# Optimization experiments

Measured on AMD Instinct MI355X. Metric: run time of the kernel, lower is better.

The kernel has to match this reference:

```python
import jax, jax.numpy as jnp
import numpy as np

B, H, W, C, F = 8, 128, 128, 256, 256

def setup_inputs() -> dict:
    key = jax.random.key(0)
    k1, k2, k3 = jax.random.split(key, 3)
    x = jax.random.normal(k1, (B, H, W, C), dtype=jnp.float32)
    style = jax.random.normal(k2, (B, 1, 1, C), dtype=jnp.float32)
    # he_uniform over fan_in = 3*3*C
    limit = np.sqrt(6.0 / (3 * 3 * C)).astype(np.float32)
    kernel = jax.random.uniform(k3, (3, 3, C, F), dtype=jnp.float32, minval=-limit, maxval=limit)
    return {"x": x, "style": style, "kernel": kernel}

def reference(x, style, kernel):
    b, h, w_, c = x.shape
    f = kernel.shape[-1]
    # per-sample modulation: [B,1,1,C,1] * [1,3,3,C,F] -> [B,3,3,C,F]
    wmod = kernel[None] * (style[..., None] + 1.0)
    demod = jnp.sqrt(jnp.sum(jnp.square(wmod), axis=(1, 2, 3), keepdims=True) + 1e-8)
    wmod = wmod / demod
    # grouped conv trick: x -> [1, B*C, H, W], filters -> [3,3,C,B*F], groups=B
    xg = jnp.transpose(x, (0, 3, 1, 2)).reshape(1, b * c, h, w_)
    wf = jnp.transpose(wmod, (1, 2, 3, 0, 4)).reshape(3, 3, c, b * f)
    y = jax.lax.conv_general_dilated(
        xg, wf, window_strides=(1, 1), padding='SAME',
        dimension_numbers=('NCHW', 'HWIO', 'NCHW'),
        feature_group_count=b)
    y = y.reshape(b, f, h, w_)
    return jnp.transpose(y, (0, 2, 3, 1))
```

## Files before the change

### kernel.cpp

```cpp
#include <hip/hip_runtime.h>
#include <hip/hip_bf16.h>


#define NB 8
#define NH 128
#define NW 128
#define NC 256
#define NF 256

typedef __attribute__((ext_vector_type(8))) short bf16x8;
typedef __attribute__((ext_vector_type(4))) float f32x4;

__global__ void k_cvt(const float* __restrict__ x, ushort* __restrict__ xbf) {
    int i = (blockIdx.x * blockDim.x + threadIdx.x) * 4;
    float4 v = *(const float4*)(x + i);
    union { ushort4 u; __hip_bfloat16 h[4]; } o;
    o.h[0] = __float2bfloat16(v.x);
    o.h[1] = __float2bfloat16(v.y);
    o.h[2] = __float2bfloat16(v.z);
    o.h[3] = __float2bfloat16(v.w);
    *(ushort4*)(xbf + i) = o.u;
}

__global__ void k_modw(const float* __restrict__ kern, const float* __restrict__ style,
                       ushort* __restrict__ wm) {
    int b = blockIdx.x >> 8;
    int f = blockIdx.x & 255;
    int c = threadIdx.x;
    float s = style[b * 256 + c] + 1.0f;
    float w[9];
    float acc = 0.f;
#pragma unroll
    for (int t = 0; t < 9; ++t) {
        w[t] = kern[(t * 256 + c) * 256 + f] * s;
        acc += w[t] * w[t];
    }
#pragma unroll
    for (int off = 32; off; off >>= 1) acc += __shfl_down(acc, off);
    __shared__ float part[4];
    if ((threadIdx.x & 63) == 0) part[threadIdx.x >> 6] = acc;
    __syncthreads();
    float total = part[0] + part[1] + part[2] + part[3];
    float inv = 1.0f / sqrtf(total + 1e-8f);
#pragma unroll
    for (int t = 0; t < 9; ++t) {
        union { ushort u; __hip_bfloat16 h; } o;
        o.h = __float2bfloat16(w[t] * inv);
        wm[(((b * 9 + t) * 256 + f) * 256) + c] = o.u;
    }
}

__global__ void __launch_bounds__(256)
k_conv(const ushort* __restrict__ xbf, const ushort* __restrict__ wm,
       float* __restrict__ out) {
    const int bidx = blockIdx.x;
    const int fh = bidx & 1;
    const int h  = (bidx >> 1) & 127;
    const int b  = bidx >> 8;

    __shared__ ushort As[3][130 * 32];
    __shared__ ushort Bs[128 * 32];

    const int tid = threadIdx.x;
    const int wave = tid >> 6, lane = tid & 63;
    const int wm_ = wave & 1, wn_ = wave >> 1;
    const int lrow = lane & 15;
    const int quad = lane >> 4;

    for (int i = tid; i < 3 * 2 * 32; i += 256) {
        int dh = i >> 6;
        int side = (i >> 5) & 1;
        int cc = i & 31;
        As[dh][(side ? 129 : 0) * 32 + cc] = 0;
    }
#pragma unroll
    for (int dh = 0; dh < 3; ++dh) {
        int hp = h + dh - 1;
        if (hp < 0 || hp >= 128) {
            for (int i = tid; i < 130 * 32; i += 256) As[dh][i] = 0;
        }
    }

    f32x4 acc[4][4];
    const f32x4 zero4 = {0.f, 0.f, 0.f, 0.f};
#pragma unroll
    for (int mi = 0; mi < 4; ++mi)
#pragma unroll
        for (int ni = 0; ni < 4; ++ni) acc[mi][ni] = zero4;

    const int wload = tid >> 2;
    const int cload = (tid & 3) * 8;

    for (int c0 = 0; c0 < 256; c0 += 32) {
        __syncthreads();
#pragma unroll
        for (int dh = 0; dh < 3; ++dh) {
            int hp = h + dh - 1;
            if (hp >= 0 && hp < 128) {
                const ushort* src = xbf + ((b * 128 + hp) * 128) * 256 + c0;
#pragma unroll
                for (int j = 0; j < 2; ++j) {
                    int w = j * 64 + wload;
                    uint4 v = *(const uint4*)(src + w * 256 + cload);
                    *(uint4*)&As[dh][(w + 1) * 32 + cload] = v;
                }
            }
        }
#pragma unroll
        for (int dh = 0; dh < 3; ++dh) {
#pragma unroll
            for (int dw = 0; dw < 3; ++dw) {
                const int tap = dh * 3 + dw;
                __syncthreads();
                {
                    const ushort* src = wm + ((b * 9 + tap) * 256 + fh * 128) * 256 + c0;
#pragma unroll
                    for (int j = 0; j < 2; ++j) {
                        int fl = j * 64 + wload;
                        uint4 v = *(const uint4*)(src + fl * 256 + cload);
                        *(uint4*)&Bs[fl * 32 + cload] = v;
                    }
                }
                __syncthreads();
                bf16x8 af[4], bfr[4];
#pragma unroll
                for (int ni = 0; ni < 4; ++ni) {
                    int fl = wn_ * 64 + ni * 16 + lrow;
                    bfr[ni] = *(const bf16x8*)&Bs[fl * 32 + quad * 8];
                }
#pragma unroll
                for (int mi = 0; mi < 4; ++mi) {
                    int w = wm_ * 64 + mi * 16 + lrow;
                    af[mi] = *(const bf16x8*)&As[dh][(w + dw) * 32 + quad * 8];
                }
#pragma unroll
                for (int mi = 0; mi < 4; ++mi)
#pragma unroll
                    for (int ni = 0; ni < 4; ++ni)
                        acc[mi][ni] = __builtin_amdgcn_mfma_f32_16x16x32_bf16(
                            af[mi], bfr[ni], acc[mi][ni], 0, 0, 0);
            }
        }
    }

    float* obase = out + ((b * 128 + h) * 128) * 256 + fh * 128;
#pragma unroll
    for (int mi = 0; mi < 4; ++mi) {
        int wrow = wm_ * 64 + mi * 16 + quad * 4;
#pragma unroll
        for (int ni = 0; ni < 4; ++ni) {
            int f = wn_ * 64 + ni * 16 + lrow;
            f32x4 v = acc[mi][ni];
#pragma unroll
            for (int r = 0; r < 4; ++r) {
                obase[(wrow + r) * 256 + f] = v[r];
            }
        }
    }
}

extern "C" void kernel_launch(void* const* d_in, const int* in_sizes, int n_in,
                              void* d_out, int out_size, void* d_ws, size_t ws_size,
                              hipStream_t stream) {
    const float* x     = (const float*)d_in[0];
    const float* style = (const float*)d_in[1];
    const float* kern  = (const float*)d_in[2];
    float* out = (float*)d_out;

    ushort* xbf = (ushort*)d_ws;
    ushort* wmod = xbf + (size_t)NB * NH * NW * NC;

    k_cvt<<<(NB * NH * NW * NC) / (256 * 4), 256, 0, stream>>>(x, xbf);
    k_modw<<<NB * NF, 256, 0, stream>>>(kern, style, wmod);
    k_conv<<<NB * NH * 2, 256, 0, stream>>>(xbf, wmod, out);
}
```

Before: 408.4 us.

## Double-buffer weight tiles with direct global-to-LDS loads and swizzle block order

Weight and input tiles are now loaded straight from global memory into LDS with global_load_lds, with no round trip through registers. The weight tile is double-buffered so the next tap's weights are prefetched while the current tap's MFMAs run, which roughly halves the barriers per channel chunk. Block indices are remapped so that consecutive launched blocks spread across batches, which changes which blocks run together and how they share cache. The risk is that the asynchronous LDS loads depend on the compiler inserting the right vmcnt waits before each barrier.

```diff
diff --git a/kernel.cpp b/kernel.cpp
--- a/kernel.cpp
+++ b/kernel.cpp
@@ -10,6 +10,12 @@
 
 typedef __attribute__((ext_vector_type(8))) short bf16x8;
 typedef __attribute__((ext_vector_type(4))) float f32x4;
+
+__device__ __forceinline__ void gload16(const ushort* g, ushort* l) {
+    __builtin_amdgcn_global_load_lds(
+        (const __attribute__((address_space(1))) unsigned int*)g,
+        (__attribute__((address_space(3))) unsigned int*)l, 16, 0, 0);
+}
 
 __global__ void k_cvt(const float* __restrict__ x, ushort* __restrict__ xbf) {
     int i = (blockIdx.x * blockDim.x + threadIdx.x) * 4;
@@ -53,19 +59,22 @@
 __global__ void __launch_bounds__(256)
 k_conv(const ushort* __restrict__ xbf, const ushort* __restrict__ wm,
        float* __restrict__ out) {
-    const int bidx = blockIdx.x;
+    const int bidx = (blockIdx.x & 7) * 256 + (blockIdx.x >> 3);
     const int fh = bidx & 1;
     const int h  = (bidx >> 1) & 127;
     const int b  = bidx >> 8;
 
     __shared__ ushort As[3][130 * 32];
-    __shared__ ushort Bs[128 * 32];
+    __shared__ ushort Bs[2][128 * 32];
 
     const int tid = threadIdx.x;
     const int wave = tid >> 6, lane = tid & 63;
     const int wm_ = wave & 1, wn_ = wave >> 1;
     const int lrow = lane & 15;
     const int quad = lane >> 4;
+
+    const int lw = lane >> 2;
+    const int lc = (lane & 3) * 8;
 
     for (int i = tid; i < 3 * 2 * 32; i += 256) {
         int dh = i >> 6;
@@ -88,62 +97,70 @@
 #pragma unroll
         for (int ni = 0; ni < 4; ++ni) acc[mi][ni] = zero4;
 
-    const int wload = tid >> 2;
-    const int cload = (tid & 3) * 8;
+    const ushort* wmb = wm + ((size_t)(b * 9) * 256 + fh * 128) * 256;
 
-    for (int c0 = 0; c0 < 256; c0 += 32) {
-        __syncthreads();
+    auto stageA = [&](int c0) {
 #pragma unroll
         for (int dh = 0; dh < 3; ++dh) {
             int hp = h + dh - 1;
             if (hp >= 0 && hp < 128) {
-                const ushort* src = xbf + ((b * 128 + hp) * 128) * 256 + c0;
+                const ushort* src = xbf + ((size_t)(b * 128 + hp) * 128) * 256 + c0;
 #pragma unroll
                 for (int j = 0; j < 2; ++j) {
-                    int w = j * 64 + wload;
-                    uint4 v = *(const uint4*)(src + w * 256 + cload);
-                    *(uint4*)&As[dh][(w + 1) * 32 + cload] = v;
+                    int w = j * 64 + wave * 16;
+                    gload16(src + (w + lw) * 256 + lc, &As[dh][(w + 1) * 32]);
                 }
             }
         }
+    };
+    auto stageB = [&](int tap, int buf, int c0) {
+        const ushort* src = wmb + tap * 65536 + c0;
 #pragma unroll
-        for (int dh = 0; dh < 3; ++dh) {
+        for (int j = 0; j < 2; ++j) {
+            int fl = j * 64 + wave * 16;
+            gload16(src + (fl + lw) * 256 + lc, &Bs[buf][fl * 32]);
+        }
+    };
+
+    stageA(0);
+    stageB(0, 0, 0);
+
+    for (int ci = 0; ci < 8; ++ci) {
+        const int c0 = ci * 32;
+        __syncthreads();
 #pragma unroll
-            for (int dw = 0; dw < 3; ++dw) {
-                const int tap = dh * 3 + dw;
-                __syncthreads();
-                {
-                    const ushort* src = wm + ((b * 9 + tap) * 256 + fh * 128) * 256 + c0;
+        for (int tap = 0; tap < 9; ++tap) {
+            const int dh = tap / 3, dw = tap % 3;
+            if (tap < 8) stageB(tap + 1, (tap + 1) & 1, c0);
+
+            bf16x8 af[4], bfr[4];
 #pragma unroll
-                    for (int j = 0; j < 2; ++j) {
-                        int fl = j * 64 + wload;
-                        uint4 v = *(const uint4*)(src + fl * 256 + cload);
-                        *(uint4*)&Bs[fl * 32 + cload] = v;
-                    }
-                }
-                __syncthreads();
-                bf16x8 af[4], bfr[4];
+            for (int ni = 0; ni < 4; ++ni) {
+                int fl = wn_ * 64 + ni * 16 + lrow;
+                bfr[ni] = *(const bf16x8*)&Bs[tap & 1][fl * 32 + quad * 8];
+            }
 #pragma unroll
-                for (int ni = 0; ni < 4; ++ni) {
-                    int fl = wn_ * 64 + ni * 16 + lrow;
-                    bfr[ni] = *(const bf16x8*)&Bs[fl * 32 + quad * 8];
-                }
+            for (int mi = 0; mi < 4; ++mi) {
+                int w = wm_ * 64 + mi * 16 + lrow;
+                af[mi] = *(const bf16x8*)&As[dh][(w + dw) * 32 + quad * 8];
+            }
 #pragma unroll
-                for (int mi = 0; mi < 4; ++mi) {
-                    int w = wm_ * 64 + mi * 16 + lrow;
-                    af[mi] = *(const bf16x8*)&As[dh][(w + dw) * 32 + quad * 8];
-                }
+            for (int mi = 0; mi < 4; ++mi)
 #pragma unroll
-                for (int mi = 0; mi < 4; ++mi)
-#pragma unroll
-                    for (int ni = 0; ni < 4; ++ni)
-                        acc[mi][ni] = __builtin_amdgcn_mfma_f32_16x16x32_bf16(
-                            af[mi], bfr[ni], acc[mi][ni], 0, 0, 0);
-            }
+                for (int ni = 0; ni < 4; ++ni)
+                    acc[mi][ni] = __builtin_amdgcn_mfma_f32_16x16x32_bf16(
+                        af[mi], bfr[ni], acc[mi][ni], 0, 0, 0);
+
+            if (tap < 8) __syncthreads();
+        }
+        if (ci < 7) {
+            __syncthreads();
+            stageA(c0 + 32);
+            stageB(0, 0, c0 + 32);
         }
     }
 
-    float* obase = out + ((b * 128 + h) * 128) * 256 + fh * 128;
+    float* obase = out + ((size_t)(b * 128 + h) * 128) * 256 + fh * 128;
 #pragma unroll
     for (int mi = 0; mi < 4; ++mi) {
         int wrow = wm_ * 64 + mi * 16 + quad * 4;
```

Measured after the change: 405.5 us. About the same (-0.7%).
